# Performance work log

Hardware: AMD Instinct MI355X
Metric: run time of the kernel (lower is better)

The kernel has to match this reference:

```python
import jax, jax.numpy as jnp
import numpy as np

N_BITS = 8  # abits = wbits = 8 (symmetric signed per-tensor quant)
QN = -2 ** (N_BITS - 1)
QP = 2 ** (N_BITS - 1) - 1


def _round_pass(v):
    # straight-through round: forward round, backward identity
    return v + jax.lax.stop_gradient(jnp.round(v) - v)


def _quantize(t):
    # per-tensor symmetric quantization; scale detached like torch .detach()
    scale = jax.lax.stop_gradient(jnp.max(jnp.abs(t))) / QP
    q = _round_pass(jnp.clip(t / scale, QN, QP))
    return q, scale


def _quantized_linear(x3, s_x, w, b):
    # x3: [B, S, Din]; w: [Dout, Din]; b: [Dout]; s_x: scalar dequant scale
    B, S, Din = x3.shape
    x2 = x3.reshape(-1, Din) * s_x              # dequantize incoming activations
    qw, sw = _quantize(w)
    qx, sx = _quantize(x2)
    out = jnp.matmul(qx, qw.T)                  # int-valued float GEMM
    out = out + b[None, :]                      # bias added before rescale (as in source)
    return (out * (sw * sx)).reshape(B, S, -1)


def setup_inputs() -> dict:
    key = jax.random.key(0)
    k1, k2, k3, k4, k5 = jax.random.split(key, 5)
    B, S, D, H = 128, 197, 384, 1536
    x = jax.random.normal(k1, (B, S, D), dtype=jnp.float32)
    act_scaling_factor = jnp.ones((1,), dtype=jnp.float32)
    w1 = jax.random.normal(k2, (H, D), dtype=jnp.float32) * (1.0 / np.sqrt(D))
    b1 = jax.random.normal(k3, (H,), dtype=jnp.float32) * 0.02
    w2 = jax.random.normal(k4, (D, H), dtype=jnp.float32) * (1.0 / np.sqrt(H))
    b2 = jax.random.normal(k5, (D,), dtype=jnp.float32) * 0.02
    return {"x": x, "act_scaling_factor": act_scaling_factor,
            "w1": w1, "b1": b1, "w2": w2, "b2": b2}


def reference(x, act_scaling_factor, w1, b1, w2, b2):
    s_x = act_scaling_factor.reshape(())
    h = _quantized_linear(x, s_x, w1, b1)       # fc1
    h = jax.nn.gelu(h, approximate=False)       # torch nn.GELU (erf)
    qh, s_h = _quantize(h)                      # qact1: requantize activations
    out = _quantized_linear(qh, s_h, w2, b2)    # fc2
    return out
```

## Files before the change

kernel.cpp:

```cpp
#include <hip/hip_runtime.h>
#include <hip/hip_bf16.h>
#include <stdint.h>
#include <math.h>

typedef int v4i __attribute__((ext_vector_type(4)));

#define GPTR(p) ((const __attribute__((address_space(1))) void*)(p))
#define LPTR(p) ((__attribute__((address_space(3))) void*)(p))

__device__ __forceinline__ float wave_max(float m) {
#pragma unroll
  for (int off = 32; off > 0; off >>= 1)
    m = fmaxf(m, __shfl_xor(m, off, 64));
  return m;
}

__device__ __forceinline__ float gelu_tanh(float x) {
  const float x2 = x * x;
  const float p = fmaf(0.044715f, x2, 1.0f);
  const float u = x * p;
  const float e = exp2f(-2.3022082f * u);
  return x * __builtin_amdgcn_rcpf(1.0f + e);
}

__global__ void absmax3_kernel(const float* __restrict__ x, int nx4,
                               const float* __restrict__ smul,
                               const float* __restrict__ w1, int nw14,
                               const float* __restrict__ w2, int nw24,
                               unsigned* __restrict__ scal) {
  __shared__ float red[4];
  const int bid = blockIdx.x;
  const float4* s4;
  int n4, b0, nb;
  float s = 1.0f;
  unsigned* dst;
  if (bid < 512)      { s4 = (const float4*)x;  n4 = nx4;  s = smul[0]; dst = scal;     b0 = bid;       nb = 512; }
  else if (bid < 640) { s4 = (const float4*)w1; n4 = nw14;              dst = scal + 1; b0 = bid - 512; nb = 128; }
  else                { s4 = (const float4*)w2; n4 = nw24;              dst = scal + 2; b0 = bid - 640; nb = 128; }
  float m = 0.0f;
  const int stride = nb * blockDim.x;
  for (int i = b0 * blockDim.x + threadIdx.x; i < n4; i += stride) {
    float4 v = s4[i];
    m = fmaxf(m, fabsf(v.x * s));
    m = fmaxf(m, fabsf(v.y * s));
    m = fmaxf(m, fabsf(v.z * s));
    m = fmaxf(m, fabsf(v.w * s));
  }
  m = wave_max(m);
  if ((threadIdx.x & 63) == 0) red[threadIdx.x >> 6] = m;
  __syncthreads();
  if (threadIdx.x == 0)
    atomicMax(dst, __float_as_uint(fmaxf(fmaxf(red[0], red[1]), fmaxf(red[2], red[3]))));
}

__global__ void quantize3_kernel(const float* __restrict__ x, int nx4,
                                 const float* __restrict__ smul,
                                 const float* __restrict__ w1, int nw14,
                                 const float* __restrict__ w2, int nw24,
                                 const unsigned* __restrict__ scal,
                                 int8_t* __restrict__ qx,
                                 int8_t* __restrict__ qw1,
                                 int8_t* __restrict__ qw2) {
  const int bid = blockIdx.x;
  const float4* s4;
  char4* d4;
  int n4, b0, nb;
  float s = 1.0f, mx;
  if (bid < 2048)      { s4 = (const float4*)x;  d4 = (char4*)qx;  n4 = nx4;  s = smul[0]; mx = __uint_as_float(scal[0]); b0 = bid;        nb = 2048; }
  else if (bid < 2176) { s4 = (const float4*)w1; d4 = (char4*)qw1; n4 = nw14;              mx = __uint_as_float(scal[1]); b0 = bid - 2048; nb = 128; }
  else                 { s4 = (const float4*)w2; d4 = (char4*)qw2; n4 = nw24;              mx = __uint_as_float(scal[2]); b0 = bid - 2176; nb = 128; }
  const float scale = mx / 127.0f;
  const int stride = nb * blockDim.x;
  for (int i = b0 * blockDim.x + threadIdx.x; i < n4; i += stride) {
    float4 v = s4[i];
    char4 qq;
    qq.x = (signed char)(int)rintf(fminf(fmaxf((v.x * s) / scale, -128.0f), 127.0f));
    qq.y = (signed char)(int)rintf(fminf(fmaxf((v.y * s) / scale, -128.0f), 127.0f));
    qq.z = (signed char)(int)rintf(fminf(fmaxf((v.z * s) / scale, -128.0f), 127.0f));
    qq.w = (signed char)(int)rintf(fminf(fmaxf((v.w * s) / scale, -128.0f), 127.0f));
    d4[i] = qq;
  }
}

__global__ void reduce_scale_kernel(const float* __restrict__ partial, int n,
                                    unsigned* __restrict__ scal) {
  __shared__ float red[4];
  float m = -3.4e38f;
  for (int i = threadIdx.x; i < n; i += blockDim.x) m = fmaxf(m, partial[i]);
  m = wave_max(m);
  if ((threadIdx.x & 63) == 0) red[threadIdx.x >> 6] = m;
  __syncthreads();
  if (threadIdx.x == 0) {
    m = fmaxf(fmaxf(red[0], red[1]), fmaxf(red[2], red[3]));
    const float sx = __uint_as_float(scal[0]) / 127.0f;
    const float sw = __uint_as_float(scal[1]) / 127.0f;
    const float max_f = m * (sw * sx);
    scal[3] = __float_as_uint(fmaxf(gelu_tanh(max_f), 0.1699702f));
  }
}

#define CBAR()                          \
  do {                                  \
    __builtin_amdgcn_sched_barrier(0);  \
    __builtin_amdgcn_s_barrier();       \
    __builtin_amdgcn_sched_barrier(0);  \
  } while (0)

template <int EPI, int BM>
__device__ __forceinline__
void gemm_body(const int8_t* __restrict__ A, const int8_t* __restrict__ B,
               const float* __restrict__ bias,
               const unsigned* __restrict__ scal,
               float* __restrict__ partial,
               int8_t* __restrict__ out_i8,
               float* __restrict__ out_f32,
               int N, int K, int GN) {
  constexpr int FR = BM / 32;
  constexpr int AH = BM / 64;
  __shared__ __align__(16) int8_t lA[2][BM * 64];
  __shared__ __align__(16) int8_t lB[2][128 * 64];

  const int nwg = gridDim.x;
  const int q = nwg >> 3, rr = nwg & 7;
  const int xcd = blockIdx.x & 7, sub = blockIdx.x >> 3;
  const int wg = (xcd < rr ? xcd * (q + 1) : rr * (q + 1) + (xcd - rr) * q) + sub;
  const int bx = wg % GN;
  const int by = wg / GN;

  const int t = threadIdx.x;
  const int lane = t & 63;
  const int wave = t >> 6;
  const int wr = wave >> 1;
  const int wc = wave & 1;
  const size_t m0 = (size_t)by * BM;
  const int n0 = bx * 128;

  const int8_t* Ab = A + m0 * (size_t)K;
  const int8_t* Bb = B + (size_t)n0 * (size_t)K;

  v4i acc[FR][4] = {};
  const int KT = K >> 6;

  const int row0 = t >> 2;
  const int ss = (t & 3) ^ ((row0 >> 1) & 3);
  const int ubase = __builtin_amdgcn_readfirstlane((t & 192) * 16);
  const size_t srcA0 = (size_t)row0 * K + (size_t)(ss * 16);
  const size_t srcA1 = (size_t)(row0 + 64) * K + (size_t)(ss * 16);

  auto stage = [&](int buf, int kt) {
    const int8_t* ga = Ab + kt * 64;
    const int8_t* gb = Bb + kt * 64;
    __builtin_amdgcn_global_load_lds(GPTR(ga + srcA0), LPTR(&lA[buf][ubase]), 16, 0, 0);
    if constexpr (AH == 2)
      __builtin_amdgcn_global_load_lds(GPTR(ga + srcA1), LPTR(&lA[buf][4096 + ubase]), 16, 0, 0);
    __builtin_amdgcn_global_load_lds(GPTR(gb + srcA0), LPTR(&lB[buf][ubase]), 16, 0, 0);
    __builtin_amdgcn_global_load_lds(GPTR(gb + srcA1), LPTR(&lB[buf][4096 + ubase]), 16, 0, 0);
  };

  const int r15 = lane & 15;
  const int q4 = lane >> 4;

  auto compute = [&](int buf) {
    v4i af[FR], bf[4];
#pragma unroll
    for (int fr = 0; fr < FR; ++fr) {
      const int row = wr * (BM / 2) + fr * 16 + r15;
      const int slot = q4 ^ ((row >> 1) & 3);
      af[fr] = *(const v4i*)(&lA[buf][row * 64 + slot * 16]);
    }
#pragma unroll
    for (int fc = 0; fc < 4; ++fc) {
      const int row = wc * 64 + fc * 16 + r15;
      const int slot = q4 ^ ((row >> 1) & 3);
      bf[fc] = *(const v4i*)(&lB[buf][row * 64 + slot * 16]);
    }
#pragma unroll
    for (int fr = 0; fr < FR; ++fr)
#pragma unroll
      for (int fc = 0; fc < 4; ++fc)
        acc[fr][fc] = __builtin_amdgcn_mfma_i32_16x16x64_i8(af[fr], bf[fc], acc[fr][fc], 0, 0, 0);
  };

  stage(0, 0);
  int cur = 0;
  for (int kt = 0; kt < KT; ++kt) {
    if (kt + 1 < KT) {
      stage(cur ^ 1, kt + 1);
      if constexpr (AH == 2) asm volatile("s_waitcnt vmcnt(4)" ::: "memory");
      else                   asm volatile("s_waitcnt vmcnt(3)" ::: "memory");
    } else {
      asm volatile("s_waitcnt vmcnt(0)" ::: "memory");
    }
    CBAR();
    compute(cur);
    if (kt + 1 < KT) {
      asm volatile("s_waitcnt lgkmcnt(0)" ::: "memory");
      CBAR();
    }
    cur ^= 1;
  }

  const int rb = q4 * 4;

  if constexpr (EPI == 0) {
    float lm = -3.4e38f;
#pragma unroll
    for (int fc = 0; fc < 4; ++fc) {
      int im = acc[0][fc][0];
#pragma unroll
      for (int fr = 0; fr < FR; ++fr)
#pragma unroll
        for (int r = 0; r < 4; ++r) im = max(im, acc[fr][fc][r]);
      const float bv = bias[n0 + wc * 64 + fc * 16 + r15];
      lm = fmaxf(lm, (float)im + bv);
    }
    lm = wave_max(lm);
    __syncthreads();
    float* red = (float*)lA;
    if (lane == 0) red[wave] = lm;
    __syncthreads();
    if (t == 0)
      partial[wg] = fmaxf(fmaxf(red[0], red[1]), fmaxf(red[2], red[3]));
  } else if constexpr (EPI == 1) {
    const float sx = __uint_as_float(scal[0]) / 127.0f;
    const float sw = __uint_as_float(scal[1]) / 127.0f;
    const float s1 = sw * sx;
    const float sh = __uint_as_float(scal[3]) / 127.0f;
    const float inv_sh = __builtin_amdgcn_rcpf(sh);
    __syncthreads();
    int8_t* qt = (int8_t*)lA;
#pragma unroll
    for (int fc = 0; fc < 4; ++fc) {
      const int col = wc * 64 + fc * 16 + r15;
      const float bv = bias[n0 + col];
      const float bvs = bv * s1;
#pragma unroll
      for (int fr = 0; fr < 4; ++fr) {
        const int rowb = wr * 64 + fr * 16 + rb;
#pragma unroll
        for (int r = 0; r < 4; ++r) {
          const float f = fmaf((float)acc[fr][fc][r], s1, bvs);
          const float g = gelu_tanh(f);
          const float qv = rintf(fminf(fmaxf(g * inv_sh, -128.0f), 127.0f));
          qt[(rowb + r) * 128 + (col ^ (q4 << 4))] = (int8_t)(int)qv;
        }
      }
    }
    __syncthreads();
#pragma unroll
    for (int v = 0; v < 4; ++v) {
      const int row = v * 32 + (t >> 3);
      const int colb = (t & 7) * 16;
      const int swz = ((row >> 2) & 3) << 4;
      *(v4i*)(out_i8 + (m0 + row) * (size_t)N + n0 + colb) =
          *(const v4i*)(qt + row * 128 + (colb ^ swz));
    }
  } else {
    const float sw2 = __uint_as_float(scal[2]) / 127.0f;
    const float sh = __uint_as_float(scal[3]) / 127.0f;
    const float x2max = 127.0f * sh;
    const float sx2 = x2max / 127.0f;
    const float s2 = sw2 * sx2;
#pragma unroll
    for (int fc = 0; fc < 4; ++fc) {
      const int n = n0 + wc * 64 + fc * 16 + r15;
      const float bv = bias[n];
      const float bvs = bv * s2;
#pragma unroll
      for (int fr = 0; fr < FR; ++fr) {
#pragma unroll
        for (int r = 0; r < 4; ++r) {
          const size_t m = m0 + (size_t)(wr * (BM / 2) + fr * 16 + rb + r);
          out_f32[m * (size_t)N + n] = fmaf((float)acc[fr][fc][r], s2, bvs);
        }
      }
    }
  }
}

__global__ __launch_bounds__(256, 4)
void gemm1_absmax_kernel(const int8_t* A, const int8_t* B, const float* bias,
                         const unsigned* scal, float* partial, int N, int K, int GN) {
  gemm_body<0, 128>(A, B, bias, scal, partial, nullptr, nullptr, N, K, GN);
}

__global__ __launch_bounds__(256, 4)
void gemm1_quant_kernel(const int8_t* A, const int8_t* B, const float* bias,
                        const unsigned* scal, int8_t* out_i8, int N, int K, int GN) {
  gemm_body<1, 128>(A, B, bias, scal, nullptr, out_i8, nullptr, N, K, GN);
}

__global__ __launch_bounds__(256, 5)
void gemm2_out_kernel(const int8_t* A, const int8_t* B, const float* bias,
                      const unsigned* scal, float* out_f32, int N, int K, int GN) {
  gemm_body<2, 64>(A, B, bias, scal, nullptr, nullptr, out_f32, N, K, GN);
}

extern "C" void kernel_launch(void* const* d_in, const int* in_sizes, int n_in,
                              void* d_out, int out_size, void* d_ws, size_t ws_size,
                              hipStream_t stream) {
  const float* x   = (const float*)d_in[0];
  const float* sxp = (const float*)d_in[1];
  const float* w1  = (const float*)d_in[2];
  const float* b1  = (const float*)d_in[3];
  const float* w2  = (const float*)d_in[4];
  const float* b2  = (const float*)d_in[5];

  const int H = in_sizes[3];
  const int D = in_sizes[5];
  const int M = in_sizes[0] / D;
  const int GM1 = M / 128;
  const int GM2 = M / 64;
  const int GN1 = H / 128;
  const int GN2 = D / 128;

  uint8_t* ws = (uint8_t*)d_ws;
  unsigned* scal = (unsigned*)ws;
  size_t off = 256;
  float* partial = (float*)(ws + off); off += 16384;
  int8_t* qx  = (int8_t*)(ws + off); off += (size_t)M * D;
  int8_t* qw1 = (int8_t*)(ws + off); off += (size_t)H * D;
  int8_t* qw2 = (int8_t*)(ws + off); off += (size_t)D * H;
  int8_t* qh  = (int8_t*)(ws + off); off += (size_t)M * H;
  (void)ws_size; (void)n_in; (void)out_size;

  hipMemsetAsync(scal, 0, 16, stream);

  absmax3_kernel<<<dim3(768), dim3(256), 0, stream>>>(
      x, M * D / 4, sxp, w1, H * D / 4, w2, D * H / 4, scal);

  quantize3_kernel<<<dim3(2304), dim3(256), 0, stream>>>(
      x, M * D / 4, sxp, w1, H * D / 4, w2, D * H / 4, scal, qx, qw1, qw2);

  dim3 blk(256);
  dim3 g1(GN1 * GM1);
  gemm1_absmax_kernel<<<g1, blk, 0, stream>>>(qx, qw1, b1, scal, partial, H, D, GN1);
  reduce_scale_kernel<<<1, 256, 0, stream>>>(partial, GM1 * GN1, scal);
  gemm1_quant_kernel<<<g1, blk, 0, stream>>>(qx, qw1, b1, scal, qh, H, D, GN1);

  dim3 g2(GN2 * GM2);
  gemm2_out_kernel<<<g2, blk, 0, stream>>>(qh, qw2, b2, scal, (float*)d_out, D, H, GN2);
}
```

Measured before the change: 135.4 us.

## Replace GEMM1 recompute with int16 spill of pre-GELU activations and separate requant pass

Instead of running the first GEMM twice (once for the global max, once to requantize), the fused path runs it once. It stores pre-GELU values as per-tile-scaled int16 in workspace and records each tile's max and abs-max. A small quanth kernel then applies GELU and int8 requantization once the global scale is known. This removes a full GEMM pass but adds a 2-byte-per-element write and read of the hidden activations, and the int16 intermediate can change rounding of the requantized values. The path is used only when the workspace is large enough.

```diff
diff --git a/kernel.cpp b/kernel.cpp
--- a/kernel.cpp
+++ b/kernel.cpp
@@ -1,9 +1,9 @@
 #include <hip/hip_runtime.h>
 #include <hip/hip_bf16.h>
 #include <stdint.h>
-#include <math.h>
 
 typedef int v4i __attribute__((ext_vector_type(4)));
+typedef int v2i __attribute__((ext_vector_type(2)));
 
 #define GPTR(p) ((const __attribute__((address_space(1))) void*)(p))
 #define LPTR(p) ((__attribute__((address_space(3))) void*)(p))
@@ -17,8 +17,7 @@
 
 __device__ __forceinline__ float gelu_tanh(float x) {
   const float x2 = x * x;
-  const float p = fmaf(0.044715f, x2, 1.0f);
-  const float u = x * p;
+  const float u = x * fmaf(0.044715f, x2, 1.0f);
   const float e = exp2f(-2.3022082f * u);
   return x * __builtin_amdgcn_rcpf(1.0f + e);
 }
@@ -83,7 +82,7 @@
 }
 
 __global__ void reduce_scale_kernel(const float* __restrict__ partial, int n,
-                                    unsigned* __restrict__ scal) {
+                                    unsigned* __restrict__ scal, int pre_scaled) {
   __shared__ float red[4];
   float m = -3.4e38f;
   for (int i = threadIdx.x; i < n; i += blockDim.x) m = fmaxf(m, partial[i]);
@@ -92,10 +91,45 @@
   __syncthreads();
   if (threadIdx.x == 0) {
     m = fmaxf(fmaxf(red[0], red[1]), fmaxf(red[2], red[3]));
-    const float sx = __uint_as_float(scal[0]) / 127.0f;
-    const float sw = __uint_as_float(scal[1]) / 127.0f;
-    const float max_f = m * (sw * sx);
+    float max_f;
+    if (pre_scaled) {
+      max_f = m;
+    } else {
+      const float sx = __uint_as_float(scal[0]) / 127.0f;
+      const float sw = __uint_as_float(scal[1]) / 127.0f;
+      max_f = m * (sw * sx);
+    }
     scal[3] = __float_as_uint(fmaxf(gelu_tanh(max_f), 0.1699702f));
+  }
+}
+
+__global__ __launch_bounds__(256)
+void quanth_kernel(const short* __restrict__ h16, const float* __restrict__ fscale,
+                   const unsigned* __restrict__ scal, int8_t* __restrict__ qh,
+                   int H, int GN) {
+  const int tile = blockIdx.x;
+  const int by = tile / GN, bx = tile % GN;
+  const size_t m0 = (size_t)by * 128;
+  const int n0 = bx * 128;
+  const float fsc = fscale[tile] * (1.0f / 32767.0f);
+  const float sh = __uint_as_float(scal[3]) / 127.0f;
+  const float inv_sh = __builtin_amdgcn_rcpf(sh);
+  const int t = threadIdx.x;
+  const int r15 = t & 15;
+#pragma unroll
+  for (int v = 0; v < 8; ++v) {
+    const int row = v * 16 + (t >> 4);
+    const size_t base = (m0 + row) * (size_t)H + n0 + r15 * 8;
+    const v4i raw = *(const v4i*)(&h16[base]);
+    const short* sp = (const short*)&raw;
+    signed char c[8];
+#pragma unroll
+    for (int j = 0; j < 8; ++j) {
+      const float f = (float)sp[j] * fsc;
+      const float g = gelu_tanh(f);
+      c[j] = (signed char)(int)rintf(fminf(fmaxf(g * inv_sh, -128.0f), 127.0f));
+    }
+    *(v2i*)(&qh[base]) = *(const v2i*)c;
   }
 }
 
@@ -111,14 +145,16 @@
 void gemm_body(const int8_t* __restrict__ A, const int8_t* __restrict__ B,
                const float* __restrict__ bias,
                const unsigned* __restrict__ scal,
-               float* __restrict__ partial,
-               int8_t* __restrict__ out_i8,
+               float* __restrict__ partial, float* __restrict__ fscale,
+               int8_t* __restrict__ out_i8, short* __restrict__ out_i16,
                float* __restrict__ out_f32,
                int N, int K, int GN) {
   constexpr int FR = BM / 32;
   constexpr int AH = BM / 64;
-  __shared__ __align__(16) int8_t lA[2][BM * 64];
-  __shared__ __align__(16) int8_t lB[2][128 * 64];
+  __shared__ __align__(16) int8_t lds[2 * BM * 64 + 2 * 128 * 64];
+  __shared__ float red8[8];
+  int8_t (*lA)[BM * 64] = (int8_t(*)[BM * 64])lds;
+  int8_t (*lB)[128 * 64] = (int8_t(*)[128 * 64])(lds + 2 * BM * 64);
 
   const int nwg = gridDim.x;
   const int q = nwg >> 3, rr = nwg & 7;
@@ -126,6 +162,7 @@
   const int wg = (xcd < rr ? xcd * (q + 1) : rr * (q + 1) + (xcd - rr) * q) + sub;
   const int bx = wg % GN;
   const int by = wg / GN;
+  const int tid0 = by * GN + bx;
 
   const int t = threadIdx.x;
   const int lane = t & 63;
@@ -215,12 +252,10 @@
       lm = fmaxf(lm, (float)im + bv);
     }
     lm = wave_max(lm);
-    __syncthreads();
-    float* red = (float*)lA;
-    if (lane == 0) red[wave] = lm;
+    if (lane == 0) red8[wave] = lm;
     __syncthreads();
     if (t == 0)
-      partial[wg] = fmaxf(fmaxf(red[0], red[1]), fmaxf(red[2], red[3]));
+      partial[tid0] = fmaxf(fmaxf(red8[0], red8[1]), fmaxf(red8[2], red8[3]));
   } else if constexpr (EPI == 1) {
     const float sx = __uint_as_float(scal[0]) / 127.0f;
     const float sw = __uint_as_float(scal[1]) / 127.0f;
@@ -228,12 +263,11 @@
     const float sh = __uint_as_float(scal[3]) / 127.0f;
     const float inv_sh = __builtin_amdgcn_rcpf(sh);
     __syncthreads();
-    int8_t* qt = (int8_t*)lA;
+    int8_t* qt = lds;
 #pragma unroll
     for (int fc = 0; fc < 4; ++fc) {
       const int col = wc * 64 + fc * 16 + r15;
-      const float bv = bias[n0 + col];
-      const float bvs = bv * s1;
+      const float bvs = bias[n0 + col] * s1;
 #pragma unroll
       for (int fr = 0; fr < 4; ++fr) {
         const int rowb = wr * 64 + fr * 16 + rb;
@@ -255,45 +289,101 @@
       *(v4i*)(out_i8 + (m0 + row) * (size_t)N + n0 + colb) =
           *(const v4i*)(qt + row * 128 + (colb ^ swz));
     }
-  } else {
+  } else if constexpr (EPI == 2) {
     const float sw2 = __uint_as_float(scal[2]) / 127.0f;
     const float sh = __uint_as_float(scal[3]) / 127.0f;
-    const float x2max = 127.0f * sh;
-    const float sx2 = x2max / 127.0f;
-    const float s2 = sw2 * sx2;
+    const float s2 = sw2 * ((127.0f * sh) / 127.0f);
 #pragma unroll
     for (int fc = 0; fc < 4; ++fc) {
       const int n = n0 + wc * 64 + fc * 16 + r15;
-      const float bv = bias[n];
-      const float bvs = bv * s2;
-#pragma unroll
-      for (int fr = 0; fr < FR; ++fr) {
+      const float bvs = bias[n] * s2;
+#pragma unroll
+      for (int fr = 0; fr < FR; ++fr)
 #pragma unroll
         for (int r = 0; r < 4; ++r) {
           const size_t m = m0 + (size_t)(wr * (BM / 2) + fr * 16 + rb + r);
           out_f32[m * (size_t)N + n] = fmaf((float)acc[fr][fc][r], s2, bvs);
         }
+    }
+  } else {
+    const float sx = __uint_as_float(scal[0]) / 127.0f;
+    const float sw = __uint_as_float(scal[1]) / 127.0f;
+    const float s1 = sw * sx;
+    float fmax_ = -3.4e38f, famax_ = 0.0f;
+#pragma unroll
+    for (int fc = 0; fc < 4; ++fc) {
+      const float bvs = bias[n0 + wc * 64 + fc * 16 + r15] * s1;
+#pragma unroll
+      for (int fr = 0; fr < 4; ++fr)
+#pragma unroll
+        for (int r = 0; r < 4; ++r) {
+          const float f = fmaf((float)acc[fr][fc][r], s1, bvs);
+          fmax_ = fmaxf(fmax_, f);
+          famax_ = fmaxf(famax_, fabsf(f));
+        }
+    }
+#pragma unroll
+    for (int off = 32; off > 0; off >>= 1) {
+      fmax_ = fmaxf(fmax_, __shfl_xor(fmax_, off, 64));
+      famax_ = fmaxf(famax_, __shfl_xor(famax_, off, 64));
+    }
+    __syncthreads();
+    if (lane == 0) { red8[wave] = fmax_; red8[4 + wave] = famax_; }
+    __syncthreads();
+    const float bfmax = fmaxf(fmaxf(red8[0], red8[1]), fmaxf(red8[2], red8[3]));
+    const float F = fmaxf(fmaxf(fmaxf(red8[4], red8[5]), fmaxf(red8[6], red8[7])), 1e-20f);
+    if (t == 0) { partial[tid0] = bfmax; fscale[tid0] = F; }
+    const float inv = 32767.0f / F;
+    short* qt16 = (short*)lds;
+#pragma unroll
+    for (int fc = 0; fc < 4; ++fc) {
+      const int col = wc * 64 + fc * 16 + r15;
+      const float bvs = bias[n0 + col] * s1;
+#pragma unroll
+      for (int fr = 0; fr < 4; ++fr) {
+        const int rowb = wr * 64 + fr * 16 + rb;
+#pragma unroll
+        for (int r = 0; r < 4; ++r) {
+          const float f = fmaf((float)acc[fr][fc][r], s1, bvs);
+          qt16[(rowb + r) * 128 + (col ^ (q4 << 4))] = (short)(int)rintf(f * inv);
+        }
       }
     }
-  }
+    __syncthreads();
+#pragma unroll
+    for (int v = 0; v < 8; ++v) {
+      const int row = v * 16 + (t >> 4);
+      const int col16 = (t & 15) * 8;
+      const int swz = ((row >> 2) & 3) << 4;
+      *(v4i*)(&out_i16[(m0 + row) * (size_t)N + n0 + col16]) =
+          *(const v4i*)(&qt16[row * 128 + (col16 ^ swz)]);
+    }
+  }
+}
+
+__global__ __launch_bounds__(256, 4)
+void gemm1_fused_kernel(const int8_t* A, const int8_t* B, const float* bias,
+                        const unsigned* scal, float* partial, float* fscale,
+                        short* h16, int N, int K, int GN) {
+  gemm_body<3, 128>(A, B, bias, scal, partial, fscale, nullptr, h16, nullptr, N, K, GN);
 }
 
 __global__ __launch_bounds__(256, 4)
 void gemm1_absmax_kernel(const int8_t* A, const int8_t* B, const float* bias,
                          const unsigned* scal, float* partial, int N, int K, int GN) {
-  gemm_body<0, 128>(A, B, bias, scal, partial, nullptr, nullptr, N, K, GN);
+  gemm_body<0, 128>(A, B, bias, scal, partial, nullptr, nullptr, nullptr, nullptr, N, K, GN);
 }
 
 __global__ __launch_bounds__(256, 4)
 void gemm1_quant_kernel(const int8_t* A, const int8_t* B, const float* bias,
                         const unsigned* scal, int8_t* out_i8, int N, int K, int GN) {
-  gemm_body<1, 128>(A, B, bias, scal, nullptr, out_i8, nullptr, N, K, GN);
+  gemm_body<1, 128>(A, B, bias, scal, nullptr, nullptr, out_i8, nullptr, nullptr, N, K, GN);
 }
 
 __global__ __launch_bounds__(256, 5)
 void gemm2_out_kernel(const int8_t* A, const int8_t* B, const float* bias,
                       const unsigned* scal, float* out_f32, int N, int K, int GN) {
-  gemm_body<2, 64>(A, B, bias, scal, nullptr, nullptr, out_f32, N, K, GN);
+  gemm_body<2, 64>(A, B, bias, scal, nullptr, nullptr, nullptr, nullptr, out_f32, N, K, GN);
 }
 
 extern "C" void kernel_launch(void* const* d_in, const int* in_sizes, int n_in,
@@ -318,11 +408,15 @@
   unsigned* scal = (unsigned*)ws;
   size_t off = 256;
   float* partial = (float*)(ws + off); off += 16384;
+  float* fscale  = (float*)(ws + off); off += 16384;
   int8_t* qx  = (int8_t*)(ws + off); off += (size_t)M * D;
   int8_t* qw1 = (int8_t*)(ws + off); off += (size_t)H * D;
   int8_t* qw2 = (int8_t*)(ws + off); off += (size_t)D * H;
   int8_t* qh  = (int8_t*)(ws + off); off += (size_t)M * H;
-  (void)ws_size; (void)n_in; (void)out_size;
+  short*  h16 = (short*)(ws + off);
+  const size_t need = off + 2ull * M * H;
+  const bool fused = (ws_size >= need);
+  (void)n_in; (void)out_size;
 
   hipMemsetAsync(scal, 0, 16, stream);
 
@@ -334,9 +428,15 @@
 
   dim3 blk(256);
   dim3 g1(GN1 * GM1);
-  gemm1_absmax_kernel<<<g1, blk, 0, stream>>>(qx, qw1, b1, scal, partial, H, D, GN1);
-  reduce_scale_kernel<<<1, 256, 0, stream>>>(partial, GM1 * GN1, scal);
-  gemm1_quant_kernel<<<g1, blk, 0, stream>>>(qx, qw1, b1, scal, qh, H, D, GN1);
+  if (fused) {
+    gemm1_fused_kernel<<<g1, blk, 0, stream>>>(qx, qw1, b1, scal, partial, fscale, h16, H, D, GN1);
+    reduce_scale_kernel<<<1, 256, 0, stream>>>(partial, GM1 * GN1, scal, 1);
+    quanth_kernel<<<g1, blk, 0, stream>>>(h16, fscale, scal, qh, H, GN1);
+  } else {
+    gemm1_absmax_kernel<<<g1, blk, 0, stream>>>(qx, qw1, b1, scal, partial, H, D, GN1);
+    reduce_scale_kernel<<<1, 256, 0, stream>>>(partial, GM1 * GN1, scal, 0);
+    gemm1_quant_kernel<<<g1, blk, 0, stream>>>(qx, qw1, b1, scal, qh, H, D, GN1);
+  }
 
   dim3 g2(GN2 * GM2);
   gemm2_out_kernel<<<g2, blk, 0, stream>>>(qh, qw2, b2, scal, (float*)d_out, D, H, GN2);
```

Result: faster. 132.5 us (-2.2%).

## Keep full-K weight tile resident in LDS for fc1 GEMMs with per-wave A streaming

Applied to the files above, without the earlier changes.

Replaces the shared fc1 GEMM body with a dedicated kernel that loads the whole 128x384 int8 weight tile into padded LDS once. Each wave then streams its own 32-row A slice through a private double buffer, so the main loop needs no block-wide barriers. Each wave now covers all 128 output columns, the epilogue stages quantized tiles in per-wave LDS, and the gemm2 path is specialized to BM=64. The trade-off is about 67KB of LDS per block, which lowers occupancy to 2 blocks per CU, and more accumulator registers per wave.

```diff
diff --git a/kernel.cpp b/kernel.cpp
--- a/kernel.cpp
+++ b/kernel.cpp
@@ -1,7 +1,6 @@
 #include <hip/hip_runtime.h>
 #include <hip/hip_bf16.h>
 #include <stdint.h>
-#include <math.h>
 
 typedef int v4i __attribute__((ext_vector_type(4)));
 
@@ -17,8 +16,7 @@
 
 __device__ __forceinline__ float gelu_tanh(float x) {
   const float x2 = x * x;
-  const float p = fmaf(0.044715f, x2, 1.0f);
-  const float u = x * p;
+  const float u = x * fmaf(0.044715f, x2, 1.0f);
   const float e = exp2f(-2.3022082f * u);
   return x * __builtin_amdgcn_rcpf(1.0f + e);
 }
@@ -99,6 +97,148 @@
   }
 }
 
+template <int EPI>
+__global__ __launch_bounds__(256, 2)
+void fc1_kernel(const int8_t* __restrict__ A, const int8_t* __restrict__ B,
+                const float* __restrict__ bias, const unsigned* __restrict__ scal,
+                float* __restrict__ partial, int8_t* __restrict__ qh,
+                int N, int K, int GN) {
+  __shared__ __align__(16) int8_t lB[128 * 400];
+  __shared__ __align__(16) int8_t lAb[4 * 2 * 2048];
+  __shared__ float red8[4];
+
+  const int nwg = gridDim.x;
+  const int q = nwg >> 3, rr = nwg & 7;
+  const int xcd = blockIdx.x & 7, sub = blockIdx.x >> 3;
+  const int wg = (xcd < rr ? xcd * (q + 1) : rr * (q + 1) + (xcd - rr) * q) + sub;
+  const int bx = wg % GN;
+  const int by = wg / GN;
+  const int tid0 = by * GN + bx;
+
+  const int t = threadIdx.x;
+  const int lane = t & 63;
+  const int wave = t >> 6;
+  const int r15 = lane & 15;
+  const int q4 = lane >> 4;
+  const size_t m0 = (size_t)by * 128;
+  const int n0 = bx * 128;
+  const size_t ws0 = m0 + wave * 32;
+
+  const int8_t* Bg = B + (size_t)n0 * K;
+#pragma unroll
+  for (int i = 0; i < 12; ++i) {
+    const int chunk = i * 256 + t;
+    const int row = chunk / 24;
+    const int col = chunk - row * 24;
+    *(v4i*)(&lB[row * 400 + col * 16]) = *(const v4i*)(Bg + (size_t)chunk * 16);
+  }
+
+  size_t srcA0, srcA1;
+  {
+    const int o0 = lane * 16;
+    const int r0_ = o0 >> 6;
+    const int ss0 = ((o0 >> 4) & 3) ^ ((r0_ >> 1) & 3);
+    srcA0 = (ws0 + r0_) * (size_t)K + (size_t)(ss0 * 16);
+    const int o1 = 1024 + lane * 16;
+    const int r1_ = o1 >> 6;
+    const int ss1 = ((o1 >> 4) & 3) ^ ((r1_ >> 1) & 3);
+    srcA1 = (ws0 + r1_) * (size_t)K + (size_t)(ss1 * 16);
+  }
+  const int awbase = __builtin_amdgcn_readfirstlane(wave * 4096);
+
+  auto stageA = [&](int buf, int kt) {
+    const int8_t* g = A + kt * 64;
+    __builtin_amdgcn_global_load_lds(GPTR(g + srcA0), LPTR(&lAb[awbase + buf * 2048]), 16, 0, 0);
+    __builtin_amdgcn_global_load_lds(GPTR(g + srcA1), LPTR(&lAb[awbase + buf * 2048 + 1024]), 16, 0, 0);
+  };
+
+  int aoffc[2];
+#pragma unroll
+  for (int fr = 0; fr < 2; ++fr) {
+    const int row = fr * 16 + r15;
+    aoffc[fr] = row * 64 + ((q4 ^ ((row >> 1) & 3)) * 16);
+  }
+  const int bbase = r15 * 400 + q4 * 16;
+
+  v4i acc[2][8] = {};
+  const int KT = K >> 6;
+
+  stageA(0, 0);
+  __syncthreads();
+
+  int cur = 0;
+  for (int kt = 0; kt < KT; ++kt) {
+    if (kt + 1 < KT) {
+      stageA(cur ^ 1, kt + 1);
+      asm volatile("s_waitcnt vmcnt(2)" ::: "memory");
+    } else {
+      asm volatile("s_waitcnt vmcnt(0)" ::: "memory");
+    }
+    v4i af[2], bf[8];
+#pragma unroll
+    for (int fr = 0; fr < 2; ++fr)
+      af[fr] = *(const v4i*)(&lAb[awbase + cur * 2048 + aoffc[fr]]);
+#pragma unroll
+    for (int fc = 0; fc < 8; ++fc)
+      bf[fc] = *(const v4i*)(&lB[bbase + fc * 6400 + kt * 64]);
+#pragma unroll
+    for (int fr = 0; fr < 2; ++fr)
+#pragma unroll
+      for (int fc = 0; fc < 8; ++fc)
+        acc[fr][fc] = __builtin_amdgcn_mfma_i32_16x16x64_i8(af[fr], bf[fc], acc[fr][fc], 0, 0, 0);
+    cur ^= 1;
+  }
+
+  if constexpr (EPI == 0) {
+    float lm = -3.4e38f;
+#pragma unroll
+    for (int fc = 0; fc < 8; ++fc) {
+      int im = acc[0][fc][0];
+#pragma unroll
+      for (int fr = 0; fr < 2; ++fr)
+#pragma unroll
+        for (int r = 0; r < 4; ++r) im = max(im, acc[fr][fc][r]);
+      lm = fmaxf(lm, (float)im + bias[n0 + fc * 16 + r15]);
+    }
+    lm = wave_max(lm);
+    if (lane == 0) red8[wave] = lm;
+    __syncthreads();
+    if (t == 0)
+      partial[tid0] = fmaxf(fmaxf(red8[0], red8[1]), fmaxf(red8[2], red8[3]));
+  } else {
+    const float sx = __uint_as_float(scal[0]) / 127.0f;
+    const float sw = __uint_as_float(scal[1]) / 127.0f;
+    const float s1 = sw * sx;
+    const float sh = __uint_as_float(scal[3]) / 127.0f;
+    const float inv_sh = __builtin_amdgcn_rcpf(sh);
+    int8_t* qt = &lAb[wave * 4096];
+#pragma unroll
+    for (int fc = 0; fc < 8; ++fc) {
+      const int col = fc * 16 + r15;
+      const float bvs = bias[n0 + col] * s1;
+#pragma unroll
+      for (int fr = 0; fr < 2; ++fr) {
+        const int rowb = fr * 16 + q4 * 4;
+#pragma unroll
+        for (int r = 0; r < 4; ++r) {
+          const float f = fmaf((float)acc[fr][fc][r], s1, bvs);
+          const float g = gelu_tanh(f);
+          const float qv = rintf(fminf(fmaxf(g * inv_sh, -128.0f), 127.0f));
+          qt[(rowb + r) * 128 + (col ^ (q4 << 4))] = (int8_t)(int)qv;
+        }
+      }
+    }
+#pragma unroll
+    for (int p = 0; p < 4; ++p) {
+      const int row = p * 8 + (lane >> 3);
+      const int colb = (lane & 7) * 16;
+      const int swz = ((row >> 2) & 3) << 4;
+      *(v4i*)(qh + (ws0 + row) * (size_t)N + n0 + colb) =
+          *(const v4i*)(qt + row * 128 + (colb ^ swz));
+    }
+  }
+}
+
 #define CBAR()                          \
   do {                                  \
     __builtin_amdgcn_sched_barrier(0);  \
@@ -106,17 +246,12 @@
     __builtin_amdgcn_sched_barrier(0);  \
   } while (0)
 
-template <int EPI, int BM>
-__device__ __forceinline__
-void gemm_body(const int8_t* __restrict__ A, const int8_t* __restrict__ B,
-               const float* __restrict__ bias,
-               const unsigned* __restrict__ scal,
-               float* __restrict__ partial,
-               int8_t* __restrict__ out_i8,
-               float* __restrict__ out_f32,
-               int N, int K, int GN) {
-  constexpr int FR = BM / 32;
-  constexpr int AH = BM / 64;
+__global__ __launch_bounds__(256, 5)
+void gemm2_out_kernel(const int8_t* __restrict__ A, const int8_t* __restrict__ B,
+                      const float* __restrict__ bias, const unsigned* __restrict__ scal,
+                      float* __restrict__ out_f32, int N, int K, int GN) {
+  constexpr int BM = 64;
+  constexpr int FR = 2;
   __shared__ __align__(16) int8_t lA[2][BM * 64];
   __shared__ __align__(16) int8_t lB[2][128 * 64];
 
@@ -151,8 +286,6 @@
     const int8_t* ga = Ab + kt * 64;
     const int8_t* gb = Bb + kt * 64;
     __builtin_amdgcn_global_load_lds(GPTR(ga + srcA0), LPTR(&lA[buf][ubase]), 16, 0, 0);
-    if constexpr (AH == 2)
-      __builtin_amdgcn_global_load_lds(GPTR(ga + srcA1), LPTR(&lA[buf][4096 + ubase]), 16, 0, 0);
     __builtin_amdgcn_global_load_lds(GPTR(gb + srcA0), LPTR(&lB[buf][ubase]), 16, 0, 0);
     __builtin_amdgcn_global_load_lds(GPTR(gb + srcA1), LPTR(&lB[buf][4096 + ubase]), 16, 0, 0);
   };
@@ -186,8 +319,7 @@
   for (int kt = 0; kt < KT; ++kt) {
     if (kt + 1 < KT) {
       stage(cur ^ 1, kt + 1);
-      if constexpr (AH == 2) asm volatile("s_waitcnt vmcnt(4)" ::: "memory");
-      else                   asm volatile("s_waitcnt vmcnt(3)" ::: "memory");
+      asm volatile("s_waitcnt vmcnt(3)" ::: "memory");
     } else {
       asm volatile("s_waitcnt vmcnt(0)" ::: "memory");
     }
@@ -201,99 +333,21 @@
   }
 
   const int rb = q4 * 4;
-
-  if constexpr (EPI == 0) {
-    float lm = -3.4e38f;
-#pragma unroll
-    for (int fc = 0; fc < 4; ++fc) {
-      int im = acc[0][fc][0];
-#pragma unroll
-      for (int fr = 0; fr < FR; ++fr)
-#pragma unroll
-        for (int r = 0; r < 4; ++r) im = max(im, acc[fr][fc][r]);
-      const float bv = bias[n0 + wc * 64 + fc * 16 + r15];
-      lm = fmaxf(lm, (float)im + bv);
-    }
-    lm = wave_max(lm);
-    __syncthreads();
-    float* red = (float*)lA;
-    if (lane == 0) red[wave] = lm;
-    __syncthreads();
-    if (t == 0)
-      partial[wg] = fmaxf(fmaxf(red[0], red[1]), fmaxf(red[2], red[3]));
-  } else if constexpr (EPI == 1) {
-    const float sx = __uint_as_float(scal[0]) / 127.0f;
-    const float sw = __uint_as_float(scal[1]) / 127.0f;
-    const float s1 = sw * sx;
-    const float sh = __uint_as_float(scal[3]) / 127.0f;
-    const float inv_sh = __builtin_amdgcn_rcpf(sh);
-    __syncthreads();
-    int8_t* qt = (int8_t*)lA;
-#pragma unroll
-    for (int fc = 0; fc < 4; ++fc) {
-      const int col = wc * 64 + fc * 16 + r15;
-      const float bv = bias[n0 + col];
-      const float bvs = bv * s1;
-#pragma unroll
-      for (int fr = 0; fr < 4; ++fr) {
-        const int rowb = wr * 64 + fr * 16 + rb;
-#pragma unroll
-        for (int r = 0; r < 4; ++r) {
-          const float f = fmaf((float)acc[fr][fc][r], s1, bvs);
-          const float g = gelu_tanh(f);
-          const float qv = rintf(fminf(fmaxf(g * inv_sh, -128.0f), 127.0f));
-          qt[(rowb + r) * 128 + (col ^ (q4 << 4))] = (int8_t)(int)qv;
-        }
+  const float sw2 = __uint_as_float(scal[2]) / 127.0f;
+  const float sh = __uint_as_float(scal[3]) / 127.0f;
+  const float s2 = sw2 * ((127.0f * sh) / 127.0f);
+#pragma unroll
+  for (int fc = 0; fc < 4; ++fc) {
+    const int n = n0 + wc * 64 + fc * 16 + r15;
+    const float bvs = bias[n] * s2;
+#pragma unroll
+    for (int fr = 0; fr < FR; ++fr)
+#pragma unroll
+      for (int r = 0; r < 4; ++r) {
+        const size_t m = m0 + (size_t)(wr * (BM / 2) + fr * 16 + rb + r);
+        out_f32[m * (size_t)N + n] = fmaf((float)acc[fr][fc][r], s2, bvs);
       }
-    }
-    __syncthreads();
-#pragma unroll
-    for (int v = 0; v < 4; ++v) {
-      const int row = v * 32 + (t >> 3);
-      const int colb = (t & 7) * 16;
-      const int swz = ((row >> 2) & 3) << 4;
-      *(v4i*)(out_i8 + (m0 + row) * (size_t)N + n0 + colb) =
-          *(const v4i*)(qt + row * 128 + (colb ^ swz));
-    }
-  } else {
-    const float sw2 = __uint_as_float(scal[2]) / 127.0f;
-    const float sh = __uint_as_float(scal[3]) / 127.0f;
-    const float x2max = 127.0f * sh;
-    const float sx2 = x2max / 127.0f;
-    const float s2 = sw2 * sx2;
-#pragma unroll
-    for (int fc = 0; fc < 4; ++fc) {
-      const int n = n0 + wc * 64 + fc * 16 + r15;
-      const float bv = bias[n];
-      const float bvs = bv * s2;
-#pragma unroll
-      for (int fr = 0; fr < FR; ++fr) {
-#pragma unroll
-        for (int r = 0; r < 4; ++r) {
-          const size_t m = m0 + (size_t)(wr * (BM / 2) + fr * 16 + rb + r);
-          out_f32[m * (size_t)N + n] = fmaf((float)acc[fr][fc][r], s2, bvs);
-        }
-      }
-    }
-  }
-}
-
-__global__ __launch_bounds__(256, 4)
-void gemm1_absmax_kernel(const int8_t* A, const int8_t* B, const float* bias,
-                         const unsigned* scal, float* partial, int N, int K, int GN) {
-  gemm_body<0, 128>(A, B, bias, scal, partial, nullptr, nullptr, N, K, GN);
-}
-
-__global__ __launch_bounds__(256, 4)
-void gemm1_quant_kernel(const int8_t* A, const int8_t* B, const float* bias,
-                        const unsigned* scal, int8_t* out_i8, int N, int K, int GN) {
-  gemm_body<1, 128>(A, B, bias, scal, nullptr, out_i8, nullptr, N, K, GN);
-}
-
-__global__ __launch_bounds__(256, 5)
-void gemm2_out_kernel(const int8_t* A, const int8_t* B, const float* bias,
-                      const unsigned* scal, float* out_f32, int N, int K, int GN) {
-  gemm_body<2, 64>(A, B, bias, scal, nullptr, nullptr, out_f32, N, K, GN);
+  }
 }
 
 extern "C" void kernel_launch(void* const* d_in, const int* in_sizes, int n_in,
@@ -334,9 +388,9 @@
 
   dim3 blk(256);
   dim3 g1(GN1 * GM1);
-  gemm1_absmax_kernel<<<g1, blk, 0, stream>>>(qx, qw1, b1, scal, partial, H, D, GN1);
+  fc1_kernel<0><<<g1, blk, 0, stream>>>(qx, qw1, b1, scal, partial, nullptr, H, D, GN1);
   reduce_scale_kernel<<<1, 256, 0, stream>>>(partial, GM1 * GN1, scal);
-  gemm1_quant_kernel<<<g1, blk, 0, stream>>>(qx, qw1, b1, scal, qh, H, D, GN1);
+  fc1_kernel<1><<<g1, blk, 0, stream>>>(qx, qw1, b1, scal, nullptr, qh, H, D, GN1);
 
   dim3 g2(GN2 * GM2);
   gemm2_out_kernel<<<g2, blk, 0, stream>>>(qh, qw2, b2, scal, (float*)d_out, D, H, GN2);
```

Measured after the change: 141.8 us. 4.7% more time.

## Use 512-thread 128x128 GEMM tiles and simplify pipeline sync

Applied to the files above, without the earlier changes.

Moves all three int8 GEMMs to 512-thread workgroups of 8 waves on a 128x128 tile. Each wave now owns a 32x64 sub-tile, and every thread issues one A load and one B load per stage. The hand-tuned vmcnt waits and sched-barrier macros are replaced by a plain __syncthreads double-buffer loop. gemm2 moves from 64-row to 128-row tiles, which halves its grid, and the per-wave accumulator count drops. The aim is more waves per tile to hide latency, at the cost of less MFMA work per wave, coarser synchronisation, and fewer workgroups for gemm2.

```diff
diff --git a/kernel.cpp b/kernel.cpp
--- a/kernel.cpp
+++ b/kernel.cpp
@@ -1,7 +1,6 @@
 #include <hip/hip_runtime.h>
 #include <hip/hip_bf16.h>
 #include <stdint.h>
-#include <math.h>
 
 typedef int v4i __attribute__((ext_vector_type(4)));
 
@@ -17,8 +16,7 @@
 
 __device__ __forceinline__ float gelu_tanh(float x) {
   const float x2 = x * x;
-  const float p = fmaf(0.044715f, x2, 1.0f);
-  const float u = x * p;
+  const float u = x * fmaf(0.044715f, x2, 1.0f);
   const float e = exp2f(-2.3022082f * u);
   return x * __builtin_amdgcn_rcpf(1.0f + e);
 }
@@ -99,26 +97,15 @@
   }
 }
 
-#define CBAR()                          \
-  do {                                  \
-    __builtin_amdgcn_sched_barrier(0);  \
-    __builtin_amdgcn_s_barrier();       \
-    __builtin_amdgcn_sched_barrier(0);  \
-  } while (0)
-
-template <int EPI, int BM>
+template <int EPI>
 __device__ __forceinline__
 void gemm_body(const int8_t* __restrict__ A, const int8_t* __restrict__ B,
-               const float* __restrict__ bias,
-               const unsigned* __restrict__ scal,
-               float* __restrict__ partial,
-               int8_t* __restrict__ out_i8,
-               float* __restrict__ out_f32,
-               int N, int K, int GN) {
-  constexpr int FR = BM / 32;
-  constexpr int AH = BM / 64;
-  __shared__ __align__(16) int8_t lA[2][BM * 64];
+               const float* __restrict__ bias, const unsigned* __restrict__ scal,
+               float* __restrict__ partial, int8_t* __restrict__ out_i8,
+               float* __restrict__ out_f32, int N, int K, int GN) {
+  __shared__ __align__(16) int8_t lA[2][128 * 64];
   __shared__ __align__(16) int8_t lB[2][128 * 64];
+  __shared__ float red8[8];
 
   const int nwg = gridDim.x;
   const int q = nwg >> 3, rr = nwg & 7;
@@ -126,45 +113,42 @@
   const int wg = (xcd < rr ? xcd * (q + 1) : rr * (q + 1) + (xcd - rr) * q) + sub;
   const int bx = wg % GN;
   const int by = wg / GN;
+  const int tid0 = by * GN + bx;
 
   const int t = threadIdx.x;
   const int lane = t & 63;
   const int wave = t >> 6;
   const int wr = wave >> 1;
   const int wc = wave & 1;
-  const size_t m0 = (size_t)by * BM;
+  const size_t m0 = (size_t)by * 128;
   const int n0 = bx * 128;
 
   const int8_t* Ab = A + m0 * (size_t)K;
   const int8_t* Bb = B + (size_t)n0 * (size_t)K;
 
-  v4i acc[FR][4] = {};
+  v4i acc[2][4] = {};
   const int KT = K >> 6;
 
   const int row0 = t >> 2;
   const int ss = (t & 3) ^ ((row0 >> 1) & 3);
-  const int ubase = __builtin_amdgcn_readfirstlane((t & 192) * 16);
+  const int ubase = __builtin_amdgcn_readfirstlane(wave * 1024);
   const size_t srcA0 = (size_t)row0 * K + (size_t)(ss * 16);
-  const size_t srcA1 = (size_t)(row0 + 64) * K + (size_t)(ss * 16);
 
   auto stage = [&](int buf, int kt) {
     const int8_t* ga = Ab + kt * 64;
     const int8_t* gb = Bb + kt * 64;
     __builtin_amdgcn_global_load_lds(GPTR(ga + srcA0), LPTR(&lA[buf][ubase]), 16, 0, 0);
-    if constexpr (AH == 2)
-      __builtin_amdgcn_global_load_lds(GPTR(ga + srcA1), LPTR(&lA[buf][4096 + ubase]), 16, 0, 0);
     __builtin_amdgcn_global_load_lds(GPTR(gb + srcA0), LPTR(&lB[buf][ubase]), 16, 0, 0);
-    __builtin_amdgcn_global_load_lds(GPTR(gb + srcA1), LPTR(&lB[buf][4096 + ubase]), 16, 0, 0);
   };
 
   const int r15 = lane & 15;
   const int q4 = lane >> 4;
 
   auto compute = [&](int buf) {
-    v4i af[FR], bf[4];
-#pragma unroll
-    for (int fr = 0; fr < FR; ++fr) {
-      const int row = wr * (BM / 2) + fr * 16 + r15;
+    v4i af[2], bf[4];
+#pragma unroll
+    for (int fr = 0; fr < 2; ++fr) {
+      const int row = wr * 32 + fr * 16 + r15;
       const int slot = q4 ^ ((row >> 1) & 3);
       af[fr] = *(const v4i*)(&lA[buf][row * 64 + slot * 16]);
     }
@@ -175,30 +159,22 @@
       bf[fc] = *(const v4i*)(&lB[buf][row * 64 + slot * 16]);
     }
 #pragma unroll
-    for (int fr = 0; fr < FR; ++fr)
+    for (int fr = 0; fr < 2; ++fr)
 #pragma unroll
       for (int fc = 0; fc < 4; ++fc)
         acc[fr][fc] = __builtin_amdgcn_mfma_i32_16x16x64_i8(af[fr], bf[fc], acc[fr][fc], 0, 0, 0);
   };
 
   stage(0, 0);
+  __syncthreads();
   int cur = 0;
-  for (int kt = 0; kt < KT; ++kt) {
-    if (kt + 1 < KT) {
-      stage(cur ^ 1, kt + 1);
-      if constexpr (AH == 2) asm volatile("s_waitcnt vmcnt(4)" ::: "memory");
-      else                   asm volatile("s_waitcnt vmcnt(3)" ::: "memory");
-    } else {
-      asm volatile("s_waitcnt vmcnt(0)" ::: "memory");
-    }
-    CBAR();
+  for (int kt = 1; kt < KT; ++kt) {
+    stage(cur ^ 1, kt);
     compute(cur);
-    if (kt + 1 < KT) {
-      asm volatile("s_waitcnt lgkmcnt(0)" ::: "memory");
-      CBAR();
-    }
+    __syncthreads();
     cur ^= 1;
   }
+  compute(cur);
 
   const int rb = q4 * 4;
 
@@ -208,19 +184,20 @@
     for (int fc = 0; fc < 4; ++fc) {
       int im = acc[0][fc][0];
 #pragma unroll
-      for (int fr = 0; fr < FR; ++fr)
+      for (int fr = 0; fr < 2; ++fr)
 #pragma unroll
         for (int r = 0; r < 4; ++r) im = max(im, acc[fr][fc][r]);
-      const float bv = bias[n0 + wc * 64 + fc * 16 + r15];
-      lm = fmaxf(lm, (float)im + bv);
+      lm = fmaxf(lm, (float)im + bias[n0 + wc * 64 + fc * 16 + r15]);
     }
     lm = wave_max(lm);
+    if (lane == 0) red8[wave] = lm;
     __syncthreads();
-    float* red = (float*)lA;
-    if (lane == 0) red[wave] = lm;
-    __syncthreads();
-    if (t == 0)
-      partial[wg] = fmaxf(fmaxf(red[0], red[1]), fmaxf(red[2], red[3]));
+    if (t == 0) {
+      float bm = red8[0];
+#pragma unroll
+      for (int w = 1; w < 8; ++w) bm = fmaxf(bm, red8[w]);
+      partial[tid0] = bm;
+    }
   } else if constexpr (EPI == 1) {
     const float sx = __uint_as_float(scal[0]) / 127.0f;
     const float sw = __uint_as_float(scal[1]) / 127.0f;
@@ -232,11 +209,10 @@
 #pragma unroll
     for (int fc = 0; fc < 4; ++fc) {
       const int col = wc * 64 + fc * 16 + r15;
-      const float bv = bias[n0 + col];
-      const float bvs = bv * s1;
-#pragma unroll
-      for (int fr = 0; fr < 4; ++fr) {
-        const int rowb = wr * 64 + fr * 16 + rb;
+      const float bvs = bias[n0 + col] * s1;
+#pragma unroll
+      for (int fr = 0; fr < 2; ++fr) {
+        const int rowb = wr * 32 + fr * 16 + rb;
 #pragma unroll
         for (int r = 0; r < 4; ++r) {
           const float f = fmaf((float)acc[fr][fc][r], s1, bvs);
@@ -248,9 +224,10 @@
     }
     __syncthreads();
 #pragma unroll
-    for (int v = 0; v < 4; ++v) {
-      const int row = v * 32 + (t >> 3);
-      const int colb = (t & 7) * 16;
+    for (int v = 0; v < 2; ++v) {
+      const int idx = v * 512 + t;
+      const int row = idx >> 3;
+      const int colb = (idx & 7) * 16;
       const int swz = ((row >> 2) & 3) << 4;
       *(v4i*)(out_i8 + (m0 + row) * (size_t)N + n0 + colb) =
           *(const v4i*)(qt + row * 128 + (colb ^ swz));
@@ -258,42 +235,38 @@
   } else {
     const float sw2 = __uint_as_float(scal[2]) / 127.0f;
     const float sh = __uint_as_float(scal[3]) / 127.0f;
-    const float x2max = 127.0f * sh;
-    const float sx2 = x2max / 127.0f;
-    const float s2 = sw2 * sx2;
+    const float s2 = sw2 * ((127.0f * sh) / 127.0f);
 #pragma unroll
     for (int fc = 0; fc < 4; ++fc) {
       const int n = n0 + wc * 64 + fc * 16 + r15;
-      const float bv = bias[n];
-      const float bvs = bv * s2;
-#pragma unroll
-      for (int fr = 0; fr < FR; ++fr) {
+      const float bvs = bias[n] * s2;
+#pragma unroll
+      for (int fr = 0; fr < 2; ++fr)
 #pragma unroll
         for (int r = 0; r < 4; ++r) {
-          const size_t m = m0 + (size_t)(wr * (BM / 2) + fr * 16 + rb + r);
+          const size_t m = m0 + (size_t)(wr * 32 + fr * 16 + rb + r);
           out_f32[m * (size_t)N + n] = fmaf((float)acc[fr][fc][r], s2, bvs);
         }
-      }
-    }
-  }
-}
-
-__global__ __launch_bounds__(256, 4)
+    }
+  }
+}
+
+__global__ __launch_bounds__(512, 4)
 void gemm1_absmax_kernel(const int8_t* A, const int8_t* B, const float* bias,
                          const unsigned* scal, float* partial, int N, int K, int GN) {
-  gemm_body<0, 128>(A, B, bias, scal, partial, nullptr, nullptr, N, K, GN);
-}
-
-__global__ __launch_bounds__(256, 4)
+  gemm_body<0>(A, B, bias, scal, partial, nullptr, nullptr, N, K, GN);
+}
+
+__global__ __launch_bounds__(512, 4)
 void gemm1_quant_kernel(const int8_t* A, const int8_t* B, const float* bias,
                         const unsigned* scal, int8_t* out_i8, int N, int K, int GN) {
-  gemm_body<1, 128>(A, B, bias, scal, nullptr, out_i8, nullptr, N, K, GN);
-}
-
-__global__ __launch_bounds__(256, 5)
+  gemm_body<1>(A, B, bias, scal, nullptr, out_i8, nullptr, N, K, GN);
+}
+
+__global__ __launch_bounds__(512, 4)
 void gemm2_out_kernel(const int8_t* A, const int8_t* B, const float* bias,
                       const unsigned* scal, float* out_f32, int N, int K, int GN) {
-  gemm_body<2, 64>(A, B, bias, scal, nullptr, nullptr, out_f32, N, K, GN);
+  gemm_body<2>(A, B, bias, scal, nullptr, nullptr, out_f32, N, K, GN);
 }
 
 extern "C" void kernel_launch(void* const* d_in, const int* in_sizes, int n_in,
@@ -309,8 +282,7 @@
   const int H = in_sizes[3];
   const int D = in_sizes[5];
   const int M = in_sizes[0] / D;
-  const int GM1 = M / 128;
-  const int GM2 = M / 64;
+  const int GM = M / 128;
   const int GN1 = H / 128;
   const int GN2 = D / 128;
 
@@ -332,12 +304,12 @@
   quantize3_kernel<<<dim3(2304), dim3(256), 0, stream>>>(
       x, M * D / 4, sxp, w1, H * D / 4, w2, D * H / 4, scal, qx, qw1, qw2);
 
-  dim3 blk(256);
-  dim3 g1(GN1 * GM1);
+  dim3 blk(512);
+  dim3 g1(GN1 * GM);
   gemm1_absmax_kernel<<<g1, blk, 0, stream>>>(qx, qw1, b1, scal, partial, H, D, GN1);
-  reduce_scale_kernel<<<1, 256, 0, stream>>>(partial, GM1 * GN1, scal);
+  reduce_scale_kernel<<<1, 256, 0, stream>>>(partial, GM * GN1, scal);
   gemm1_quant_kernel<<<g1, blk, 0, stream>>>(qx, qw1, b1, scal, qh, H, D, GN1);
 
-  dim3 g2(GN2 * GM2);
+  dim3 g2(GN2 * GM);
   gemm2_out_kernel<<<g2, blk, 0, stream>>>(qh, qw2, b2, scal, (float*)d_out, D, H, GN2);
 }
```

Result: faster. 132.0 us (-2.6%).
